# Kernel tuning notes

Hardware: AMD Instinct MI355X
Metric: run time of the kernel (lower is better)

The kernel has to match this reference:

```python
import jax, jax.numpy as jnp
import numpy as np

B, S, H = 2, 2048, 2048
NH, KVH, HD = 16, 4, 128
R = 16
LORA_SCALE = 32.0 / 16.0  # lora_alpha / lora_r
ATTN_SCALE = HD ** -0.5
NEG = -1e9


def setup_inputs() -> dict:
    key = jax.random.key(0)
    ks = jax.random.split(key, 16)
    q_dim, kv_dim = NH * HD, KVH * HD
    # RoPE tables
    inv_freq = 1.0 / (10000.0 ** (jnp.arange(0, HD, 2, dtype=jnp.float32) / HD))
    ang = jnp.arange(S, dtype=jnp.float32)[:, None] * inv_freq[None, :]  # [S, HD/2]
    emb = jnp.concatenate([ang, ang], axis=-1)  # [S, HD]
    cos = jnp.broadcast_to(jnp.cos(emb)[None], (B, S, HD))
    sin = jnp.broadcast_to(jnp.sin(emb)[None], (B, S, HD))
    # additive causal mask [B,1,S,S]
    causal = jnp.triu(jnp.full((S, S), NEG, dtype=jnp.float32), k=1)
    attention_mask = jnp.broadcast_to(causal[None, None], (B, 1, S, S))
    return {
        'hidden_states': jax.random.normal(ks[0], (B, S, H), jnp.float32),
        'cos': cos,
        'sin': sin,
        'attention_mask': attention_mask,
        'q_w': jax.random.normal(ks[1], (q_dim, H), jnp.float32) * 0.02,
        'k_w': jax.random.normal(ks[2], (kv_dim, H), jnp.float32) * 0.02,
        'v_w': jax.random.normal(ks[3], (kv_dim, H), jnp.float32) * 0.02,
        'q_b': jax.random.normal(ks[4], (q_dim,), jnp.float32) * 0.02,
        'k_b': jax.random.normal(ks[5], (kv_dim,), jnp.float32) * 0.02,
        'v_b': jax.random.normal(ks[6], (kv_dim,), jnp.float32) * 0.02,
        'q_A': jax.random.normal(ks[7], (H, R), jnp.float32) * (1.0 / np.sqrt(H)),
        'q_B': jax.random.normal(ks[8], (R, q_dim), jnp.float32) * 0.02,
        'k_A': jax.random.normal(ks[9], (H, R), jnp.float32) * (1.0 / np.sqrt(H)),
        'k_B': jax.random.normal(ks[10], (R, kv_dim), jnp.float32) * 0.02,
        'v_A': jax.random.normal(ks[11], (H, R), jnp.float32) * (1.0 / np.sqrt(H)),
        'v_B': jax.random.normal(ks[12], (R, kv_dim), jnp.float32) * 0.02,
        'o_w': jax.random.normal(ks[13], (H, H), jnp.float32) * 0.02,
    }


def _rotate_half(x):
    x1, x2 = x[..., : HD // 2], x[..., HD // 2:]
    return jnp.concatenate([-x2, x1], axis=-1)


def reference(hidden_states, cos, sin, attention_mask,
              q_w, k_w, v_w, q_b, k_b, v_b,
              q_A, q_B, k_A, k_B, v_A, v_B, o_w):
    x = hidden_states  # dropout p=0 (eval)
    # fused base + LoRA projections
    q = x @ q_w.T + q_b + LORA_SCALE * ((x @ q_A) @ q_B)  # [B,S,NH*HD]
    k = x @ k_w.T + k_b + LORA_SCALE * ((x @ k_A) @ k_B)  # [B,S,KVH*HD]
    v = x @ v_w.T + v_b + LORA_SCALE * ((x @ v_A) @ v_B)
    q = q.reshape(B, S, NH, HD).transpose(0, 2, 1, 3)   # [B,NH,S,HD]
    k = k.reshape(B, S, KVH, HD).transpose(0, 2, 1, 3)  # [B,KVH,S,HD]
    v = v.reshape(B, S, KVH, HD).transpose(0, 2, 1, 3)
    # RoPE
    c = cos[:, None]  # [B,1,S,HD]
    s = sin[:, None]
    q = q * c + _rotate_half(q) * s
    k = k * c + _rotate_half(k) * s
    # GQA: repeat kv heads
    n_rep = NH // KVH
    k = jnp.repeat(k, n_rep, axis=1)  # [B,NH,S,HD]
    v = jnp.repeat(v, n_rep, axis=1)
    scores = jnp.einsum('bhqd,bhkd->bhqk', q, k) * ATTN_SCALE
    scores = scores + attention_mask
    attn = jax.nn.softmax(scores.astype(jnp.float32), axis=-1).astype(q.dtype)
    out = jnp.einsum('bhqk,bhkd->bhqd', attn, v)
    out = out.transpose(0, 2, 1, 3).reshape(B, S, NH * HD)  # [B,S,H]
    return out @ o_w.T
```

## Files before the change

kernel.cpp:

```cpp
#include <hip/hip_runtime.h>

constexpr int cB   = 2;
constexpr int cS   = 2048;
constexpr int cH   = 2048;
constexpr int cNH  = 16;
constexpr int cKVH = 4;
constexpr int cHD  = 128;
constexpr int cQD  = 2048;
constexpr int cKVD = 512;
constexpr int cNQKV = 3072;
constexpr int cNTOK = 4096;
#define ATTN_SCALE 0.08838834764831845f
#define QSCALE 0.12751589549581288f

typedef __bf16 bf16;
typedef __attribute__((ext_vector_type(8))) __bf16 bf16x8;
typedef __attribute__((ext_vector_type(4))) __bf16 bf16x4;
typedef __attribute__((ext_vector_type(4))) float  f32x4;

__device__ __forceinline__ void async_load16(const bf16* g, bf16* l) {
    __builtin_amdgcn_global_load_lds(
        (const __attribute__((address_space(1))) void*)g,
        (__attribute__((address_space(3))) void*)l, 16, 0, 0);
}

__global__ __launch_bounds__(256) void prep_all(
        const float* __restrict__ x, bf16* __restrict__ Xbf,
        const float* __restrict__ ow, bf16* __restrict__ OWbf,
        const float* __restrict__ qw, const float* __restrict__ kw, const float* __restrict__ vw,
        const float* __restrict__ qA, const float* __restrict__ qB,
        const float* __restrict__ kA, const float* __restrict__ kB,
        const float* __restrict__ vA, const float* __restrict__ vB,
        const float* __restrict__ qb, const float* __restrict__ kbias, const float* __restrict__ vb,
        bf16* __restrict__ Wc, float* __restrict__ biasc) {
    const int bid = blockIdx.x;
    if (bid < 8192) {
        const int i = (bid * 256 + threadIdx.x) * 4;
        f32x4 v = *(const f32x4*)(x + i);
        bf16x4 o;
        o[0] = (bf16)v[0]; o[1] = (bf16)v[1]; o[2] = (bf16)v[2]; o[3] = (bf16)v[3];
        *(bf16x4*)(Xbf + i) = o;
        return;
    }
    if (bid < 12288) {
        const int i = ((bid - 8192) * 256 + threadIdx.x) * 4;
        f32x4 v = *(const f32x4*)(ow + i);
        bf16x4 o;
        o[0] = (bf16)v[0]; o[1] = (bf16)v[1]; o[2] = (bf16)v[2]; o[3] = (bf16)v[3];
        *(bf16x4*)(OWbf + i) = o;
        return;
    }
    const int pb = bid - 12288;
    const int bx = pb & 3, by = pb >> 2;
    const int wave = threadIdx.x >> 6, lane = threadIdx.x & 63;
    const int n = by * 4 + wave;
    const int k0 = bx * 512 + lane * 8;
    const float* W; const float* Am; const float* Bm; const float* bias; int nn, nd;
    if (n < cQD)             { W = qw; Am = qA; Bm = qB; bias = qb;    nn = n;               nd = cQD; }
    else if (n < cQD + cKVD) { W = kw; Am = kA; Bm = kB; bias = kbias; nn = n - cQD;         nd = cKVD; }
    else                     { W = vw; Am = vA; Bm = vB; bias = vb;    nn = n - cQD - cKVD;  nd = cKVD; }
    if (bx == 0 && lane == 0) biasc[n] = bias[nn];
    float bm[16];
    #pragma unroll
    for (int r = 0; r < 16; ++r) bm[r] = Bm[r * nd + nn];
    const float* wrow = W + (size_t)nn * cH + k0;
    f32x4 w0 = *(const f32x4*)(wrow);
    f32x4 w1 = *(const f32x4*)(wrow + 4);
    bf16x8 o;
    #pragma unroll
    for (int j = 0; j < 8; ++j) {
        const f32x4* am = (const f32x4*)(Am + (size_t)(k0 + j) * 16);
        f32x4 a0 = am[0], a1 = am[1], a2 = am[2], a3 = am[3];
        float acc = 0.f;
        #pragma unroll
        for (int c = 0; c < 4; ++c) acc += a0[c] * bm[c] + a1[c] * bm[4 + c]
                                         + a2[c] * bm[8 + c] + a3[c] * bm[12 + c];
        const float wv = (j < 4) ? w0[j] : w1[j - 4];
        o[j] = (bf16)(wv + 2.0f * acc);
    }
    *(bf16x8*)&Wc[(size_t)n * cH + k0] = o;
}

__global__ __launch_bounds__(512, 4) void gemm_qkv6(const bf16* __restrict__ A, const bf16* __restrict__ Bw,
                                                    const float* __restrict__ bias,
                                                    const float* __restrict__ cosb, const float* __restrict__ sinb,
                                                    bf16* __restrict__ Qr, bf16* __restrict__ Kr,
                                                    bf16* __restrict__ Vt) {
    __shared__ bf16 Al[256 * 64];
    __shared__ bf16 Bl[128 * 64];
    const int tid = threadIdx.x;
    const int wave = tid >> 6, lane = tid & 63;
    const int quad = lane >> 4, l16 = lane & 15;
    const int wm = wave >> 1, wn = wave & 1;
    const int K = cH;
    constexpr int GX = cNQKV / 128;
    constexpr int NWG = GX * (cNTOK / 256);

    const int orig = blockIdx.y * GX + blockIdx.x;
    const int swz = (orig & 7) * (NWG >> 3) + (orig >> 3);
    const long bm = (long)(swz / GX) * 256;
    const long bn = (long)(swz % GX) * 128;

    f32x4 acc[4][4];
    #pragma unroll
    for (int i = 0; i < 4; ++i)
        #pragma unroll
        for (int c = 0; c < 4; ++c) acc[i][c] = f32x4{0.f, 0.f, 0.f, 0.f};

    int aago[4], aslo[4], bgo[2], bslo[2];
    #pragma unroll
    for (int i2 = 0; i2 < 4; ++i2) {
        const int si = i2 * 512 + tid;
        const int row = si >> 3, c8 = si & 7;
        aago[i2] = row * K + (c8 ^ (row & 7)) * 8;
        aslo[i2] = si * 8;
    }
    #pragma unroll
    for (int i2 = 0; i2 < 2; ++i2) {
        const int si = i2 * 512 + tid;
        const int row = si >> 3, c8 = si & 7;
        bgo[i2] = row * K + (c8 ^ (row & 7)) * 8;
        bslo[i2] = si * 8;
    }
    const size_t bmK = (size_t)bm * K, bnK = (size_t)bn * K;

    auto STAGE = [&](int tt) {
        const bf16* As_ = A  + bmK + (size_t)tt * 64;
        const bf16* Bs_ = Bw + bnK + (size_t)tt * 64;
        #pragma unroll
        for (int i2 = 0; i2 < 4; ++i2) async_load16(As_ + aago[i2], &Al[aslo[i2]]);
        #pragma unroll
        for (int i2 = 0; i2 < 2; ++i2) async_load16(Bs_ + bgo[i2], &Bl[bslo[i2]]);
    };

    constexpr int NT = cH / 64;
    STAGE(0);
    const int sw = l16 & 7;

    for (int t = 0; t < NT; ++t) {
        asm volatile("s_waitcnt vmcnt(0)" ::: "memory");
        __builtin_amdgcn_s_barrier();
        #pragma unroll
        for (int ks = 0; ks < 2; ++ks) {
            const int g = ks * 4 + quad;
            const int cofs = (g ^ sw) * 8;
            bf16x8 af[4], bfr[4];
            #pragma unroll
            for (int i = 0; i < 4; ++i)
                af[i] = *(const bf16x8*)&Al[(wm * 64 + i * 16 + l16) * 64 + cofs];
            #pragma unroll
            for (int c = 0; c < 4; ++c) {
                const int nrow = wn * 32 + (c & 1) * 16 + (c >> 1) * 64 + l16;
                bfr[c] = *(const bf16x8*)&Bl[nrow * 64 + cofs];
            }
            __builtin_amdgcn_s_setprio(1);
            #pragma unroll
            for (int i = 0; i < 4; ++i)
                #pragma unroll
                for (int c = 0; c < 4; ++c)
                    acc[i][c] = __builtin_amdgcn_mfma_f32_16x16x32_bf16(af[i], bfr[c], acc[i][c], 0, 0, 0);
            __builtin_amdgcn_s_setprio(0);
        }
        asm volatile("s_waitcnt lgkmcnt(0)" ::: "memory");
        __builtin_amdgcn_s_barrier();
        if (t + 1 < NT) STAGE(t + 1);
    }

    #pragma unroll
    for (int c = 0; c < 4; ++c) {
        const int nloc = wn * 32 + (c & 1) * 16 + (c >> 1) * 64 + l16;
        const float bv = bias[bn + nloc];
        #pragma unroll
        for (int i = 0; i < 4; ++i)
            #pragma unroll
            for (int r = 0; r < 4; ++r) acc[i][c][r] += bv;
    }

    const int head = (int)(bn >> 7);
    if (head < cNH + cKVH) {
        const bool isQ = head < cNH;
        #pragma unroll
        for (int cl = 0; cl < 2; ++cl) {
            const int d = wn * 32 + cl * 16 + l16;
            #pragma unroll
            for (int i = 0; i < 4; ++i)
                #pragma unroll
                for (int r = 0; r < 4; ++r) {
                    const long t = bm + wm * 64 + i * 16 + quad * 4 + r;
                    const float cv = cosb[t * cHD + d];
                    const float sv = sinb[t * cHD + d];
                    const float v1 = acc[i][cl][r], v2 = acc[i][cl + 2][r];
                    float o1 = v1 * cv - v2 * sv;
                    float o2 = v2 * cv + v1 * sv;
                    if (isQ) { o1 *= QSCALE; o2 *= QSCALE; }
                    const int b = (int)(t >> 11), s = (int)(t & 2047);
                    bf16* dst = isQ
                        ? Qr + ((size_t)(b * cNH + head) * cS + s) * cHD
                        : Kr + ((size_t)(b * cKVH + (head - cNH)) * cS + s) * cHD;
                    dst[d]      = (bf16)o1;
                    dst[d + 64] = (bf16)o2;
                }
        }
    } else {
        const int kv = head - cNH - cKVH;
        const int b = (int)(bm >> 11);
        const int sbase = (int)(bm & 2047);
        #pragma unroll
        for (int c = 0; c < 4; ++c) {
            const int d = wn * 32 + (c & 1) * 16 + (c >> 1) * 64 + l16;
            #pragma unroll
            for (int i = 0; i < 4; ++i) {
                const int s0 = sbase + wm * 64 + i * 16 + quad * 4;
                bf16x4 o4;
                #pragma unroll
                for (int r = 0; r < 4; ++r) o4[r] = (bf16)acc[i][c][r];
                *(bf16x4*)&Vt[((size_t)((b * cKVH + kv) * cHD) + d) * cS + s0] = o4;
            }
        }
    }
}

__global__ __launch_bounds__(256, 2) void gemm_oproj5(const bf16* __restrict__ A, const bf16* __restrict__ Bw,
                                                      float* __restrict__ Cp) {
    __shared__ bf16 Al[128 * 128];
    __shared__ bf16 Bl[128 * 128];
    const int tid = threadIdx.x;
    const int wave = tid >> 6, lane = tid & 63;
    const int quad = lane >> 4, l16 = lane & 15;
    const int wr = wave >> 1, wc = wave & 1;
    constexpr int K = cH, N = cH;
    constexpr int GX = cH / 128;
    constexpr int NWG = GX * (cNTOK / 128);

    const int orig = blockIdx.y * GX + blockIdx.x;
    const int swz = (orig & 7) * (NWG >> 3) + (orig >> 3);
    const long bm = (long)(swz / GX) * 128;
    const long bn = (long)(swz % GX) * 128;

    f32x4 acc[4][4];
    #pragma unroll
    for (int i = 0; i < 4; ++i)
        #pragma unroll
        for (int c = 0; c < 4; ++c) acc[i][c] = f32x4{0.f, 0.f, 0.f, 0.f};

    int ago[8], slo[8];
    #pragma unroll
    for (int i2 = 0; i2 < 8; ++i2) {
        const int si = i2 * 256 + tid;
        const int row = si >> 4, c16 = si & 15;
        const int csw = (c16 & 8) | ((c16 & 7) ^ (row & 7));
        ago[i2] = row * K + csw * 8;
        slo[i2] = si * 8;
    }
    const size_t bmK = (size_t)bm * K, bnK = (size_t)bn * K;

    auto STAGE = [&](int tt) {
        const bf16* As_ = A  + bmK + (size_t)tt * 128;
        const bf16* Bs_ = Bw + bnK + (size_t)tt * 128;
        #pragma unroll
        for (int i2 = 0; i2 < 8; ++i2) {
            async_load16(As_ + ago[i2], &Al[slo[i2]]);
            async_load16(Bs_ + ago[i2], &Bl[slo[i2]]);
        }
    };

    constexpr int NT = K / 128;
    STAGE(0);
    const int sw = l16 & 7;

    for (int t = 0; t < NT; ++t) {
        asm volatile("s_waitcnt vmcnt(0)" ::: "memory");
        __builtin_amdgcn_s_barrier();
        #pragma unroll
        for (int ks = 0; ks < 4; ++ks) {
            const int g = ks * 4 + quad;
            const int gsw = (g & 8) | ((g & 7) ^ sw);
            const int cofs = gsw * 8;
            bf16x8 af[4], bfr[4];
            #pragma unroll
            for (int i = 0; i < 4; ++i)
                af[i] = *(const bf16x8*)&Al[(wr * 64 + i * 16 + l16) * 128 + cofs];
            #pragma unroll
            for (int c = 0; c < 4; ++c)
                bfr[c] = *(const bf16x8*)&Bl[(wc * 64 + c * 16 + l16) * 128 + cofs];
            __builtin_amdgcn_s_setprio(1);
            #pragma unroll
            for (int i = 0; i < 4; ++i)
                #pragma unroll
                for (int c = 0; c < 4; ++c)
                    acc[i][c] = __builtin_amdgcn_mfma_f32_16x16x32_bf16(af[i], bfr[c], acc[i][c], 0, 0, 0);
            __builtin_amdgcn_s_setprio(0);
        }
        asm volatile("s_waitcnt lgkmcnt(0)" ::: "memory");
        __builtin_amdgcn_s_barrier();
        if (t + 1 < NT) STAGE(t + 1);
    }

    #pragma unroll
    for (int i = 0; i < 4; ++i)
        #pragma unroll
        for (int c = 0; c < 4; ++c) {
            const long m0 = bm + wr * 64 + i * 16 + quad * 4;
            const long n  = bn + wc * 64 + c * 16 + l16;
            #pragma unroll
            for (int r = 0; r < 4; ++r)
                Cp[(m0 + r) * N + n] = acc[i][c][r];
        }
}

__global__ __launch_bounds__(256, 2) void flash6(const bf16* __restrict__ Q, const bf16* __restrict__ K,
                                                 const bf16* __restrict__ Vt, bf16* __restrict__ Ob) {
    __shared__ bf16 kb[128 * 128];
    __shared__ bf16 vb[128 * 128];
    __shared__ bf16 pb[4 * 2048];
    const int tid = threadIdx.x;
    const int wave = tid >> 6, lane = tid & 63;
    const int quad = lane >> 4, l16 = lane & 15;
    const int pi = blockIdx.x;
    const int h = blockIdx.y, b = blockIdx.z;

    const bf16* Qh = Q  + (size_t)(b * cNH + h) * cS * cHD;
    const bf16* Kg = K  + (size_t)(b * cKVH + (h >> 2)) * cS * cHD;
    const bf16* Vg = Vt + (size_t)(b * cKVH + (h >> 2)) * cHD * cS;

    int kgo[8], vgo[8], slo[8];
    #pragma unroll
    for (int i2 = 0; i2 < 8; ++i2) {
        const int si = i2 * 256 + tid;
        const int row = si >> 4, c16 = si & 15;
        const int csw = (c16 & 8) | ((c16 & 7) ^ (row & 7));
        kgo[i2] = row * cHD + csw * 8;
        vgo[i2] = row * cS  + csw * 8;
        slo[i2] = si * 8;
    }

    #pragma unroll
    for (int t2 = 0; t2 < 2; ++t2) {
        const int qt = t2 == 0 ? (31 - pi) : pi;

        const bf16* Qg = Qh + (size_t)qt * 64 * cHD;
        bf16x8 qf[4];
        #pragma unroll
        for (int ks = 0; ks < 4; ++ks)
            qf[ks] = *(const bf16x8*)(Qg + (size_t)(wave * 16 + l16) * cHD + ks * 32 + quad * 8);

        f32x4 oac[8];
        #pragma unroll
        for (int dt = 0; dt < 8; ++dt) oac[dt] = f32x4{0.f, 0.f, 0.f, 0.f};
        float m_ = -3.0e38f, l_ = 0.f;

        const int nkt = (qt >> 1) + 1;
        for (int kt = 0; kt < nkt; ++kt) {
            __syncthreads();
            const bf16* Kt  = Kg + (size_t)kt * 128 * cHD;
            const bf16* Vtt = Vg + kt * 128;
            #pragma unroll
            for (int i2 = 0; i2 < 8; ++i2) async_load16(Kt + kgo[i2], kb + slo[i2]);
            #pragma unroll
            for (int i2 = 0; i2 < 8; ++i2) async_load16(Vtt + vgo[i2], vb + slo[i2]);
            __syncthreads();

            f32x4 st[8];
            #pragma unroll
            for (int mt = 0; mt < 8; ++mt) {
                bf16x8 kf[4];
                #pragma unroll
                for (int ks = 0; ks < 4; ++ks) {
                    const int c = ks * 4 + quad;
                    const int csw = (c & 8) | ((c & 7) ^ (l16 & 7));
                    kf[ks] = *(const bf16x8*)&kb[(mt * 16 + l16) * 128 + csw * 8];
                }
                f32x4 a = f32x4{0.f, 0.f, 0.f, 0.f};
                __builtin_amdgcn_s_setprio(1);
                #pragma unroll
                for (int ks = 0; ks < 4; ++ks)
                    a = __builtin_amdgcn_mfma_f32_16x16x32_bf16(kf[ks], qf[ks], a, 0, 0, 0);
                __builtin_amdgcn_s_setprio(0);
                st[mt] = a;
            }

            const int qpos = qt * 64 + wave * 16 + l16;
            float tmax = -3.0e38f;
            if ((kt * 128 + 127) > (qt * 64 + wave * 16)) {
                #pragma unroll
                for (int mt = 0; mt < 8; ++mt)
                    #pragma unroll
                    for (int r = 0; r < 4; ++r) {
                        const int kpos = kt * 128 + mt * 16 + quad * 4 + r;
                        if (kpos > qpos) st[mt][r] = -3.0e38f;
                        tmax = fmaxf(tmax, st[mt][r]);
                    }
            } else {
                #pragma unroll
                for (int mt = 0; mt < 8; ++mt)
                    #pragma unroll
                    for (int r = 0; r < 4; ++r) tmax = fmaxf(tmax, st[mt][r]);
            }
            tmax = fmaxf(tmax, __shfl_xor(tmax, 16, 64));
            tmax = fmaxf(tmax, __shfl_xor(tmax, 32, 64));
            const float mnew = fmaxf(m_, tmax);
            if (__any(tmax > m_)) {
                const float alpha = __builtin_amdgcn_exp2f(m_ - mnew);
                l_ *= alpha;
                #pragma unroll
                for (int dt = 0; dt < 8; ++dt)
                    #pragma unroll
                    for (int r = 0; r < 4; ++r) oac[dt][r] *= alpha;
            }
            m_ = mnew;
            float rs = 0.f;
            #pragma unroll
            for (int mt = 0; mt < 8; ++mt)
                #pragma unroll
                for (int r = 0; r < 4; ++r) {
                    const float p = __builtin_amdgcn_exp2f(st[mt][r] - mnew);
                    st[mt][r] = p;
                    rs += p;
                }
            rs += __shfl_xor(rs, 16, 64);
            rs += __shfl_xor(rs, 32, 64);
            l_ += rs;

            #pragma unroll
            for (int mt = 0; mt < 8; ++mt) {
                bf16x4 p4;
                #pragma unroll
                for (int r = 0; r < 4; ++r) p4[r] = (bf16)st[mt][r];
                const int c16 = mt * 2 + (quad >> 1);
                const int csw = (c16 & 8) | ((c16 & 7) ^ (l16 & 7));
                *(bf16x4*)&pb[wave * 2048 + l16 * 128 + csw * 8 + (quad & 1) * 4] = p4;
            }

            bf16x8 pf[4];
            #pragma unroll
            for (int ks = 0; ks < 4; ++ks) {
                const int c = ks * 4 + quad;
                const int csw = (c & 8) | ((c & 7) ^ (l16 & 7));
                pf[ks] = *(const bf16x8*)&pb[wave * 2048 + l16 * 128 + csw * 8];
            }
            #pragma unroll
            for (int dt = 0; dt < 8; ++dt) {
                bf16x8 vf[4];
                #pragma unroll
                for (int ks = 0; ks < 4; ++ks) {
                    const int c = ks * 4 + quad;
                    const int csw = (c & 8) | ((c & 7) ^ (l16 & 7));
                    vf[ks] = *(const bf16x8*)&vb[(dt * 16 + l16) * 128 + csw * 8];
                }
                __builtin_amdgcn_s_setprio(1);
                #pragma unroll
                for (int ks = 0; ks < 4; ++ks)
                    oac[dt] = __builtin_amdgcn_mfma_f32_16x16x32_bf16(vf[ks], pf[ks], oac[dt], 0, 0, 0);
                __builtin_amdgcn_s_setprio(0);
            }
        }

        const float inv = 1.0f / l_;
        const int token = qt * 64 + wave * 16 + l16;
        bf16* orow = Ob + (size_t)(b * cS + token) * (cNH * cHD) + h * cHD;
        #pragma unroll
        for (int dt = 0; dt < 8; ++dt) {
            bf16x4 o4;
            #pragma unroll
            for (int r = 0; r < 4; ++r) o4[r] = (bf16)(oac[dt][r] * inv);
            *(bf16x4*)&orow[dt * 16 + quad * 4] = o4;
        }
    }
}

extern "C" void kernel_launch(void* const* d_in, const int* in_sizes, int n_in,
                              void* d_out, int out_size, void* d_ws, size_t ws_size,
                              hipStream_t stream) {
    const float* x    = (const float*)d_in[0];
    const float* cosb = (const float*)d_in[1];
    const float* sinb = (const float*)d_in[2];
    const float* qw = (const float*)d_in[4];
    const float* kw = (const float*)d_in[5];
    const float* vw = (const float*)d_in[6];
    const float* qb = (const float*)d_in[7];
    const float* kb_ = (const float*)d_in[8];
    const float* vb = (const float*)d_in[9];
    const float* qA = (const float*)d_in[10];
    const float* qB = (const float*)d_in[11];
    const float* kA = (const float*)d_in[12];
    const float* kB = (const float*)d_in[13];
    const float* vA = (const float*)d_in[14];
    const float* vB = (const float*)d_in[15];
    const float* ow = (const float*)d_in[16];
    float* out = (float*)d_out;

    char* ws = (char*)d_ws;
    bf16* Xbf   = (bf16*)ws;  ws += (size_t)cNTOK * cH * 2;
    bf16* Wc    = (bf16*)ws;  ws += (size_t)cNQKV * cH * 2;
    float* biasc = (float*)ws; ws += (size_t)cNQKV * 4;
    bf16* Qr    = (bf16*)ws;  ws += (size_t)cB * cNH * cS * cHD * 2;
    bf16* Kr    = (bf16*)ws;  ws += (size_t)cB * cKVH * cS * cHD * 2;
    bf16* Vt    = (bf16*)ws;  ws += (size_t)cB * cKVH * cHD * cS * 2;
    bf16* OWbf  = (bf16*)ws;  ws += (size_t)cH * cH * 2;
    bf16* Aout  = (bf16*)ws;  ws += (size_t)cNTOK * cQD * 2;

    prep_all<<<15360, 256, 0, stream>>>(x, Xbf, ow, OWbf, qw, kw, vw, qA, qB, kA, kB, vA, vB,
                                        qb, kb_, vb, Wc, biasc);

    gemm_qkv6<<<dim3(cNQKV / 128, cNTOK / 256), 512, 0, stream>>>(Xbf, Wc, biasc, cosb, sinb, Qr, Kr, Vt);

    flash6<<<dim3(16, cNH, cB), 256, 0, stream>>>(Qr, Kr, Vt, Aout);

    gemm_oproj5<<<dim3(cH / 128, cNTOK / 128), 256, 0, stream>>>(Aout, OWbf, out);
}
```

Measured before the change: 361.5 us.

## Retile output projection to 256x128 with 512 threads, split flash LDS into halves

The output projection GEMM moves from 128x128 tiles with 256 threads and K-step 128 to 256x128 tiles with 512 threads and K-step 64. It uses an 8-column XOR swizzle and interleaves the N columns per wave. The flash attention kernel stores K, V and P tiles in LDS as two 64-column halves with a simpler 8-way XOR swizzle, and each wave now loads contiguous row groups. The intent is more data reuse per workgroup and fewer LDS bank conflicts, at the cost of twice as many barrier iterations in the GEMM and higher register pressure under launch_bounds(512,4).

After: 368.5 us. About the same (+1.9%).

```diff
diff --git a/kernel.cpp b/kernel.cpp
--- a/kernel.cpp
+++ b/kernel.cpp
@@ -220,21 +220,21 @@
     }
 }
 
-__global__ __launch_bounds__(256, 2) void gemm_oproj5(const bf16* __restrict__ A, const bf16* __restrict__ Bw,
+__global__ __launch_bounds__(512, 4) void gemm_oproj6(const bf16* __restrict__ A, const bf16* __restrict__ Bw,
                                                       float* __restrict__ Cp) {
-    __shared__ bf16 Al[128 * 128];
-    __shared__ bf16 Bl[128 * 128];
+    __shared__ bf16 Al[256 * 64];
+    __shared__ bf16 Bl[128 * 64];
     const int tid = threadIdx.x;
     const int wave = tid >> 6, lane = tid & 63;
     const int quad = lane >> 4, l16 = lane & 15;
-    const int wr = wave >> 1, wc = wave & 1;
+    const int wm = wave >> 1, wn = wave & 1;
     constexpr int K = cH, N = cH;
     constexpr int GX = cH / 128;
-    constexpr int NWG = GX * (cNTOK / 128);
+    constexpr int NWG = GX * (cNTOK / 256);
 
     const int orig = blockIdx.y * GX + blockIdx.x;
     const int swz = (orig & 7) * (NWG >> 3) + (orig >> 3);
-    const long bm = (long)(swz / GX) * 128;
+    const long bm = (long)(swz / GX) * 256;
     const long bn = (long)(swz % GX) * 128;
 
     f32x4 acc[4][4];
@@ -243,28 +243,33 @@
         #pragma unroll
         for (int c = 0; c < 4; ++c) acc[i][c] = f32x4{0.f, 0.f, 0.f, 0.f};
 
-    int ago[8], slo[8];
-    #pragma unroll
-    for (int i2 = 0; i2 < 8; ++i2) {
-        const int si = i2 * 256 + tid;
-        const int row = si >> 4, c16 = si & 15;
-        const int csw = (c16 & 8) | ((c16 & 7) ^ (row & 7));
-        ago[i2] = row * K + csw * 8;
-        slo[i2] = si * 8;
+    int aago[4], aslo[4], bgo[2], bslo[2];
+    #pragma unroll
+    for (int i2 = 0; i2 < 4; ++i2) {
+        const int si = i2 * 512 + tid;
+        const int row = si >> 3, c8 = si & 7;
+        aago[i2] = row * K + (c8 ^ (row & 7)) * 8;
+        aslo[i2] = si * 8;
+    }
+    #pragma unroll
+    for (int i2 = 0; i2 < 2; ++i2) {
+        const int si = i2 * 512 + tid;
+        const int row = si >> 3, c8 = si & 7;
+        bgo[i2] = row * K + (c8 ^ (row & 7)) * 8;
+        bslo[i2] = si * 8;
     }
     const size_t bmK = (size_t)bm * K, bnK = (size_t)bn * K;
 
     auto STAGE = [&](int tt) {
-        const bf16* As_ = A  + bmK + (size_t)tt * 128;
-        const bf16* Bs_ = Bw + bnK + (size_t)tt * 128;
-        #pragma unroll
-        for (int i2 = 0; i2 < 8; ++i2) {
-            async_load16(As_ + ago[i2], &Al[slo[i2]]);
-            async_load16(Bs_ + ago[i2], &Bl[slo[i2]]);
-        }
+        const bf16* As_ = A  + bmK + (size_t)tt * 64;
+        const bf16* Bs_ = Bw + bnK + (size_t)tt * 64;
+        #pragma unroll
+        for (int i2 = 0; i2 < 4; ++i2) async_load16(As_ + aago[i2], &Al[aslo[i2]]);
+        #pragma unroll
+        for (int i2 = 0; i2 < 2; ++i2) async_load16(Bs_ + bgo[i2], &Bl[bslo[i2]]);
     };
 
-    constexpr int NT = K / 128;
+    constexpr int NT = K / 64;
     STAGE(0);
     const int sw = l16 & 7;
 
@@ -272,17 +277,18 @@
         asm volatile("s_waitcnt vmcnt(0)" ::: "memory");
         __builtin_amdgcn_s_barrier();
         #pragma unroll
-        for (int ks = 0; ks < 4; ++ks) {
+        for (int ks = 0; ks < 2; ++ks) {
             const int g = ks * 4 + quad;
-            const int gsw = (g & 8) | ((g & 7) ^ sw);
-            const int cofs = gsw * 8;
+            const int cofs = (g ^ sw) * 8;
             bf16x8 af[4], bfr[4];
             #pragma unroll
             for (int i = 0; i < 4; ++i)
-                af[i] = *(const bf16x8*)&Al[(wr * 64 + i * 16 + l16) * 128 + cofs];
-            #pragma unroll
-            for (int c = 0; c < 4; ++c)
-                bfr[c] = *(const bf16x8*)&Bl[(wc * 64 + c * 16 + l16) * 128 + cofs];
+                af[i] = *(const bf16x8*)&Al[(wm * 64 + i * 16 + l16) * 64 + cofs];
+            #pragma unroll
+            for (int c = 0; c < 4; ++c) {
+                const int nrow = wn * 32 + (c & 1) * 16 + (c >> 1) * 64 + l16;
+                bfr[c] = *(const bf16x8*)&Bl[nrow * 64 + cofs];
+            }
             __builtin_amdgcn_s_setprio(1);
             #pragma unroll
             for (int i = 0; i < 4; ++i)
@@ -297,21 +303,22 @@
     }
 
     #pragma unroll
-    for (int i = 0; i < 4; ++i)
-        #pragma unroll
-        for (int c = 0; c < 4; ++c) {
-            const long m0 = bm + wr * 64 + i * 16 + quad * 4;
-            const long n  = bn + wc * 64 + c * 16 + l16;
+    for (int c = 0; c < 4; ++c) {
+        const int nloc = wn * 32 + (c & 1) * 16 + (c >> 1) * 64 + l16;
+        #pragma unroll
+        for (int i = 0; i < 4; ++i) {
+            const long m0 = bm + wm * 64 + i * 16 + quad * 4;
             #pragma unroll
             for (int r = 0; r < 4; ++r)
-                Cp[(m0 + r) * N + n] = acc[i][c][r];
-        }
+                Cp[(m0 + r) * N + bn + nloc] = acc[i][c][r];
+        }
+    }
 }
 
-__global__ __launch_bounds__(256, 2) void flash6(const bf16* __restrict__ Q, const bf16* __restrict__ K,
+__global__ __launch_bounds__(256, 2) void flash8(const bf16* __restrict__ Q, const bf16* __restrict__ K,
                                                  const bf16* __restrict__ Vt, bf16* __restrict__ Ob) {
-    __shared__ bf16 kb[128 * 128];
-    __shared__ bf16 vb[128 * 128];
+    __shared__ bf16 kb[2 * 128 * 64];
+    __shared__ bf16 vb[2 * 128 * 64];
     __shared__ bf16 pb[4 * 2048];
     const int tid = threadIdx.x;
     const int wave = tid >> 6, lane = tid & 63;
@@ -326,12 +333,14 @@
     int kgo[8], vgo[8], slo[8];
     #pragma unroll
     for (int i2 = 0; i2 < 8; ++i2) {
-        const int si = i2 * 256 + tid;
-        const int row = si >> 4, c16 = si & 15;
-        const int csw = (c16 & 8) | ((c16 & 7) ^ (row & 7));
-        kgo[i2] = row * cHD + csw * 8;
-        vgo[i2] = row * cS  + csw * 8;
-        slo[i2] = si * 8;
+        const int half = wave & 1;
+        const int row8 = i2 * 2 + (wave >> 1);
+        const int row  = row8 * 8 + (lane >> 3);
+        const int c8   = lane & 7;
+        const int gc   = half * 8 + (c8 ^ (lane >> 3));
+        kgo[i2] = row * cHD + gc * 8;
+        vgo[i2] = row * cS  + gc * 8;
+        slo[i2] = half * 8192 + row8 * 512 + lane * 8;
     }
 
     #pragma unroll
@@ -367,8 +376,8 @@
                 #pragma unroll
                 for (int ks = 0; ks < 4; ++ks) {
                     const int c = ks * 4 + quad;
-                    const int csw = (c & 8) | ((c & 7) ^ (l16 & 7));
-                    kf[ks] = *(const bf16x8*)&kb[(mt * 16 + l16) * 128 + csw * 8];
+                    kf[ks] = *(const bf16x8*)&kb[(c >> 3) * 8192 + (mt * 16 + l16) * 64
+                                                 + ((c & 7) ^ (l16 & 7)) * 8];
                 }
                 f32x4 a = f32x4{0.f, 0.f, 0.f, 0.f};
                 __builtin_amdgcn_s_setprio(1);
@@ -427,16 +436,16 @@
                 #pragma unroll
                 for (int r = 0; r < 4; ++r) p4[r] = (bf16)st[mt][r];
                 const int c16 = mt * 2 + (quad >> 1);
-                const int csw = (c16 & 8) | ((c16 & 7) ^ (l16 & 7));
-                *(bf16x4*)&pb[wave * 2048 + l16 * 128 + csw * 8 + (quad & 1) * 4] = p4;
+                *(bf16x4*)&pb[wave * 2048 + (c16 >> 3) * 1024 + l16 * 64
+                              + ((c16 & 7) ^ (l16 & 7)) * 8 + (quad & 1) * 4] = p4;
             }
 
             bf16x8 pf[4];
             #pragma unroll
             for (int ks = 0; ks < 4; ++ks) {
                 const int c = ks * 4 + quad;
-                const int csw = (c & 8) | ((c & 7) ^ (l16 & 7));
-                pf[ks] = *(const bf16x8*)&pb[wave * 2048 + l16 * 128 + csw * 8];
+                pf[ks] = *(const bf16x8*)&pb[wave * 2048 + (c >> 3) * 1024 + l16 * 64
+                                             + ((c & 7) ^ (l16 & 7)) * 8];
             }
             #pragma unroll
             for (int dt = 0; dt < 8; ++dt) {
@@ -444,8 +453,8 @@
                 #pragma unroll
                 for (int ks = 0; ks < 4; ++ks) {
                     const int c = ks * 4 + quad;
-                    const int csw = (c & 8) | ((c & 7) ^ (l16 & 7));
-                    vf[ks] = *(const bf16x8*)&vb[(dt * 16 + l16) * 128 + csw * 8];
+                    vf[ks] = *(const bf16x8*)&vb[(c >> 3) * 8192 + (dt * 16 + l16) * 64
+                                                 + ((c & 7) ^ (l16 & 7)) * 8];
                 }
                 __builtin_amdgcn_s_setprio(1);
                 #pragma unroll
@@ -504,7 +513,7 @@
 
     gemm_qkv6<<<dim3(cNQKV / 128, cNTOK / 256), 512, 0, stream>>>(Xbf, Wc, biasc, cosb, sinb, Qr, Kr, Vt);
 
-    flash6<<<dim3(16, cNH, cB), 256, 0, stream>>>(Qr, Kr, Vt, Aout);
-
-    gemm_oproj5<<<dim3(cH / 128, cNTOK / 128), 256, 0, stream>>>(Aout, OWbf, out);
+    flash8<<<dim3(16, cNH, cB), 256, 0, stream>>>(Qr, Kr, Vt, Aout);
+
+    gemm_oproj6<<<dim3(cH / 128, cNTOK / 256), 512, 0, stream>>>(Aout, OWbf, out);
 }
```
